# Kernel tuning notes

Hardware: AMD Instinct MI355X
Metric: run time of the kernel (lower is better)

Reference implementation:

```python
import jax, jax.numpy as jnp
import numpy as np

N = 50000          # nodes
E = 600000         # edges
D_IN = 256         # input_feat_dim
H1 = 128           # hidden_dim1
H2 = 64            # hidden_dim2
DK = 64            # trs_depth (total key/value depth)
HEADS = 2


def setup_inputs() -> dict:
    key = jax.random.key(0)
    ks = jax.random.split(key, 12)
    inp = {
        "ns_emb": jax.random.normal(ks[0], (N, D_IN), dtype=jnp.float32),
        "edge_rows": jax.random.randint(ks[1], (E,), 0, N, dtype=jnp.int32),
        "edge_cols": jax.random.randint(ks[2], (E,), 0, N, dtype=jnp.int32),
        "edge_vals": jax.random.uniform(ks[3], (E,), dtype=jnp.float32),
        "condition": jax.random.normal(ks[4], (1, 128, H1), dtype=jnp.float32),
        # GCN linear weights (bias=False), stored [in, out]
        "W_hidden": jax.random.normal(ks[5], (D_IN, H1), dtype=jnp.float32) / np.sqrt(D_IN),
        "W_mu": jax.random.normal(ks[6], (H1, H2), dtype=jnp.float32) / np.sqrt(H1),
        "W_var": jax.random.normal(ks[7], (H1, H2), dtype=jnp.float32) / np.sqrt(H1),
        # MultiHeadAttention (bias-free) projections
        "Wq": jax.random.normal(ks[8], (H1, DK), dtype=jnp.float32) / np.sqrt(H1),
        "Wk": jax.random.normal(ks[9], (H1, DK), dtype=jnp.float32) / np.sqrt(H1),
        "Wv": jax.random.normal(ks[10], (H1, DK), dtype=jnp.float32) / np.sqrt(H1),
        "Wo": jax.random.normal(ks[11], (DK, H1), dtype=jnp.float32) / np.sqrt(DK),
    }
    return inp


def _spmm(rows, cols, vals, x):
    # sparse [N,N] @ x  via gather + segment-sum over COO edges
    gathered = vals[:, None] * x[cols]            # [E, d]
    return jax.ops.segment_sum(gathered, rows, num_segments=N)


def _gcn(x, W, rows, cols, vals):
    # dropout is identity in eval mode
    support = jax.nn.leaky_relu(x @ W)            # [N, out]
    out = _spmm(rows, cols, vals, support)        # [N, out]
    return jax.nn.leaky_relu(out)


def _mha(q, kv, Wq, Wk, Wv, Wo):
    # MoEL-style MultiHeadAttention, bias-free, no mask/dropout
    B, Lq, _ = q.shape
    Lk = kv.shape[1]
    dk = DK // HEADS
    Q = (q @ Wq).reshape(B, Lq, HEADS, dk).transpose(0, 2, 1, 3) * (dk ** -0.5)
    K = (kv @ Wk).reshape(B, Lk, HEADS, dk).transpose(0, 2, 1, 3)
    V = (kv @ Wv).reshape(B, Lk, HEADS, dk).transpose(0, 2, 1, 3)
    logits = jnp.einsum("bhqd,bhkd->bhqk", Q, K)
    w = jax.nn.softmax(logits, axis=-1)
    ctx = jnp.einsum("bhqk,bhkd->bhqd", w, V)
    ctx = ctx.transpose(0, 2, 1, 3).reshape(B, Lq, DK)
    return ctx @ Wo, w


def reference(ns_emb, edge_rows, edge_cols, edge_vals, condition,
              W_hidden, W_mu, W_var, Wq, Wk, Wv, Wo):
    hidden = _gcn(ns_emb, W_hidden, edge_rows, edge_cols, edge_vals)   # [N, H1]
    attended, _ = _mha(hidden[None], condition, Wq, Wk, Wv, Wo)        # [1, N, H1]
    h = attended[0]
    mu = _gcn(h, W_mu, edge_rows, edge_cols, edge_vals)                # [N, H2]
    var = _gcn(h, W_var, edge_rows, edge_cols, edge_vals)              # [N, H2]
    return mu, var
```

## Files before the change

kernel.cpp:

```cpp
#include <hip/hip_runtime.h>
#include <hip/hip_bf16.h>
#include <cstdint>


typedef __attribute__((ext_vector_type(8))) short short8;
typedef __attribute__((ext_vector_type(4))) float f32x4;
typedef __attribute__((ext_vector_type(4))) unsigned short ushort4_t;

__device__ __forceinline__ unsigned short f2bf(float f) {
    unsigned int u = __builtin_bit_cast(unsigned int, f);
    u += 0x7fffu + ((u >> 16) & 1u);
    return (unsigned short)(u >> 16);
}
__device__ __forceinline__ float bf2f(unsigned short v) {
    return __builtin_bit_cast(float, (unsigned int)v << 16);
}


__global__ void hist_kernel(const int* __restrict__ rows, int* __restrict__ cnt, int E) {
    int i = blockIdx.x * blockDim.x + threadIdx.x;
    if (i < E) atomicAdd(&cnt[rows[i]], 1);
}

__global__ void scan1_kernel(const int* __restrict__ cnt, int* __restrict__ excl,
                             int* __restrict__ bsum, int N) {
    __shared__ int sh[256];
    int t = threadIdx.x;
    int i = blockIdx.x * 256 + t;
    int v = (i < N) ? cnt[i] : 0;
    sh[t] = v;
    __syncthreads();
    for (int off = 1; off < 256; off <<= 1) {
        int x = (t >= off) ? sh[t - off] : 0;
        __syncthreads();
        sh[t] += x;
        __syncthreads();
    }
    if (i < N) excl[i] = sh[t] - v;
    if (t == 255) bsum[blockIdx.x] = sh[255];
}

__global__ void scan23_kernel(const int* __restrict__ excl, const int* __restrict__ bsum,
                              int* __restrict__ row_start, int* __restrict__ cursor,
                              int nb, int N, int E) {
    __shared__ int sh[256];
    int t = threadIdx.x;
    int v = (t < nb) ? bsum[t] : 0;
    sh[t] = v;
    __syncthreads();
    for (int off = 1; off < 256; off <<= 1) {
        int x = (t >= off) ? sh[t - off] : 0;
        __syncthreads();
        sh[t] += x;
        __syncthreads();
    }
    int boff = (blockIdx.x > 0) ? sh[blockIdx.x - 1] : 0;
    int i = blockIdx.x * 256 + t;
    if (i < N) {
        int w = excl[i] + boff;
        row_start[i] = w;
        cursor[i] = w;
    }
    if (i == 0) row_start[N] = E;
}

__global__ void scatter_kernel(const int* __restrict__ rows, const int* __restrict__ colsIn,
                               const float* __restrict__ valsIn, int* __restrict__ cursor,
                               int2* __restrict__ pack, int E) {
    int i = blockIdx.x * blockDim.x + threadIdx.x;
    if (i < E) {
        int r = rows[i];
        int p = atomicAdd(&cursor[r], 1);
        pack[p] = make_int2(colsIn[i], __float_as_int(valsIn[i]));
    }
}


__global__ __launch_bounds__(256) void prep_kv_kernel(
    const float* __restrict__ Wh, const float* __restrict__ Wq,
    const float* __restrict__ Wo, const float* __restrict__ Wmu,
    const float* __restrict__ Wvar, const float* __restrict__ cond,
    const float* __restrict__ Wk, const float* __restrict__ Wv,
    unsigned short* __restrict__ WhT, unsigned short* __restrict__ WqT,
    unsigned short* __restrict__ WoT, unsigned short* __restrict__ WmuT,
    unsigned short* __restrict__ WvarT, unsigned short* __restrict__ Ktt,
    unsigned short* __restrict__ Vt)
{
    const int t = threadIdx.x;
    if (blockIdx.x < 256) {
        int idx = blockIdx.x * 256 + t;
        if (idx < 32768) {
            int n = idx & 127, k = idx >> 7;
            WhT[n * 256 + k] = f2bf(Wh[k * 128 + n]);
        } else if (idx < 40960) {
            int i = idx - 32768, n = i & 63, k = i >> 6;
            WqT[n * 128 + k] = f2bf(Wq[k * 64 + n]);
        } else if (idx < 49152) {
            int i = idx - 40960, n = i & 127, k = i >> 7;
            WoT[n * 64 + k] = f2bf(Wo[k * 128 + n]);
        } else if (idx < 57344) {
            int i = idx - 49152, n = i & 63, k = i >> 6;
            WmuT[n * 128 + k] = f2bf(Wmu[k * 64 + n]);
        } else if (idx < 65536) {
            int i = idx - 57344, n = i & 63, k = i >> 6;
            WvarT[n * 128 + k] = f2bf(Wvar[k * 64 + n]);
        }
    } else {
        int b2 = blockIdx.x - 256;
        __shared__ float c[2][128];
        c[t >> 7][t & 127] = cond[b2 * 256 + t];
        __syncthreads();
        int j = b2 * 2 + (t >> 7);
        int tl = t & 127;
        const float* W = (tl < 64) ? Wk : Wv;
        int col = tl & 63;
        float acc = 0.f;
#pragma unroll 8
        for (int k = 0; k < 128; ++k) acc = fmaf(c[t >> 7][k], W[k * 64 + col], acc);
        int h = col >> 5, d = col & 31;
        if (tl < 64) Ktt[((size_t)h * 128 + j) * 32 + d] = f2bf(acc * 0.17677669529663687f);
        else         Vt[((size_t)h * 32 + d) * 128 + j] = f2bf(acc);
    }
}


__global__ __launch_bounds__(256) void gcn1_gemm(
    const float* __restrict__ A, const unsigned short* __restrict__ BT,
    unsigned short* __restrict__ C, int M)
{
    __shared__ unsigned short As[128][72];
    __shared__ unsigned short Bs[128][72];

    const int tid = threadIdx.x;
    const int lane = tid & 63, wave = tid >> 6;
    const int wm = wave & 1, wn = wave >> 1;
    const int quad = lane >> 4, l16 = lane & 15;
    const int r0 = blockIdx.x * 128;

    f32x4 acc[4][4];
#pragma unroll
    for (int mt = 0; mt < 4; ++mt)
#pragma unroll
        for (int nt = 0; nt < 4; ++nt)
#pragma unroll
            for (int r = 0; r < 4; ++r) acc[mt][nt][r] = 0.f;

    for (int kc = 0; kc < 256; kc += 64) {
#pragma unroll
        for (int i = 0; i < 8; ++i) {
            int f = tid + 256 * i;
            int row = f >> 4, kq = (f & 15) << 2;
            int gr = r0 + row;
            if (gr >= M) gr = M - 1;
            float4 v = *reinterpret_cast<const float4*>(&A[(size_t)gr * 256 + kc + kq]);
            ushort4_t pv;
            pv[0] = f2bf(v.x); pv[1] = f2bf(v.y); pv[2] = f2bf(v.z); pv[3] = f2bf(v.w);
            *reinterpret_cast<ushort4_t*>(&As[row][kq]) = pv;
        }
#pragma unroll
        for (int i = 0; i < 4; ++i) {
            int f = tid + 256 * i;
            int n = f >> 3, k8 = (f & 7) << 3;
            *reinterpret_cast<short8*>(&Bs[n][k8]) =
                *reinterpret_cast<const short8*>(&BT[(size_t)n * 256 + kc + k8]);
        }
        __syncthreads();

#pragma unroll
        for (int ks = 0; ks < 2; ++ks) {
            const int koff = ks * 32 + quad * 8;
            short8 a[4], b[4];
#pragma unroll
            for (int mt = 0; mt < 4; ++mt)
                a[mt] = *reinterpret_cast<const short8*>(&As[wm * 64 + mt * 16 + l16][koff]);
#pragma unroll
            for (int nt = 0; nt < 4; ++nt)
                b[nt] = *reinterpret_cast<const short8*>(&Bs[wn * 64 + nt * 16 + l16][koff]);
#pragma unroll
            for (int mt = 0; mt < 4; ++mt)
#pragma unroll
                for (int nt = 0; nt < 4; ++nt)
                    acc[mt][nt] = __builtin_amdgcn_mfma_f32_16x16x32_bf16(
                        a[mt], b[nt], acc[mt][nt], 0, 0, 0);
        }
        __syncthreads();
    }

#pragma unroll
    for (int mt = 0; mt < 4; ++mt)
#pragma unroll
        for (int nt = 0; nt < 4; ++nt) {
            int gc = wn * 64 + nt * 16 + l16;
#pragma unroll
            for (int r = 0; r < 4; ++r) {
                int gr = r0 + wm * 64 + mt * 16 + quad * 4 + r;
                if (gr < M) {
                    float v = acc[mt][nt][r];
                    v = v > 0.f ? v : 0.01f * v;
                    C[(size_t)gr * 128 + gc] = f2bf(v);
                }
            }
        }
}


__global__ __launch_bounds__(256) void attn_muvar_kernel(
    const unsigned short* __restrict__ hidden,
    const unsigned short* __restrict__ WqT,
    const unsigned short* __restrict__ Ktt,
    const unsigned short* __restrict__ Vt,
    const unsigned short* __restrict__ WoT,
    const unsigned short* __restrict__ WmuT,
    const unsigned short* __restrict__ WvarT,
    unsigned short* __restrict__ muvar,
    int M)
{
    __shared__ unsigned short Ap[128 * 136];
    __shared__ unsigned short Bp[10240];
    __shared__ unsigned short Cp[128 * 72];
    __shared__ float redm[2][128];
    __shared__ float reds[2][128];

    const int tid = threadIdx.x;
    const int lane = tid & 63, wave = tid >> 6;
    const int wm = wave & 1, wn = wave >> 1;
    const int quad = lane >> 4, l16 = lane & 15;
    const int r0 = blockIdx.x * 128;

#pragma unroll
    for (int i = 0; i < 8; ++i) {
        int f = tid + 256 * i;
        int row = f >> 4, k8 = (f & 15) << 3;
        int gr = r0 + row;
        if (gr >= M) gr = M - 1;
        *reinterpret_cast<short8*>(&Ap[row * 136 + k8]) =
            *reinterpret_cast<const short8*>(&hidden[(size_t)gr * 128 + k8]);
    }
#pragma unroll
    for (int i = 0; i < 4; ++i) {
        int f = tid + 256 * i;
        int n = f >> 4, k8 = (f & 15) << 3;
        *reinterpret_cast<short8*>(&Bp[n * 136 + k8]) =
            *reinterpret_cast<const short8*>(&WqT[(size_t)n * 128 + k8]);
    }
    __syncthreads();

    {
        f32x4 accq[4][2];
#pragma unroll
        for (int mt = 0; mt < 4; ++mt)
#pragma unroll
            for (int nt = 0; nt < 2; ++nt)
#pragma unroll
                for (int r = 0; r < 4; ++r) accq[mt][nt][r] = 0.f;
#pragma unroll
        for (int ks = 0; ks < 4; ++ks) {
            const int koff = ks * 32 + quad * 8;
            short8 a[4], b[2];
#pragma unroll
            for (int mt = 0; mt < 4; ++mt)
                a[mt] = *reinterpret_cast<const short8*>(&Ap[(wm * 64 + mt * 16 + l16) * 136 + koff]);
#pragma unroll
            for (int nt = 0; nt < 2; ++nt)
                b[nt] = *reinterpret_cast<const short8*>(&Bp[(wn * 32 + nt * 16 + l16) * 136 + koff]);
#pragma unroll
            for (int mt = 0; mt < 4; ++mt)
#pragma unroll
                for (int nt = 0; nt < 2; ++nt)
                    accq[mt][nt] = __builtin_amdgcn_mfma_f32_16x16x32_bf16(
                        a[mt], b[nt], accq[mt][nt], 0, 0, 0);
        }
#pragma unroll
        for (int mt = 0; mt < 4; ++mt)
#pragma unroll
            for (int nt = 0; nt < 2; ++nt) {
                int col = wn * 32 + nt * 16 + l16;
#pragma unroll
                for (int r = 0; r < 4; ++r) {
                    int row = wm * 64 + mt * 16 + quad * 4 + r;
                    Cp[row * 72 + col] = f2bf(accq[mt][nt][r]);
                }
            }
    }
    __syncthreads();

    for (int h = 0; h < 2; ++h) {
#pragma unroll
        for (int i = 0; i < 2; ++i) {
            int f = tid + 256 * i;
            int key = f >> 2, d8 = (f & 3) << 3;
            *reinterpret_cast<short8*>(&Bp[key * 40 + d8]) =
                *reinterpret_cast<const short8*>(&Ktt[((size_t)h * 128 + key) * 32 + d8]);
        }
#pragma unroll
        for (int i = 0; i < 2; ++i) {
            int f = tid + 256 * i;
            int d = f >> 4, k8 = (f & 15) << 3;
            *reinterpret_cast<short8*>(&Bp[5120 + d * 136 + k8]) =
                *reinterpret_cast<const short8*>(&Vt[((size_t)h * 32 + d) * 128 + k8]);
        }
        __syncthreads();

        f32x4 accl[4][4];
        {
            short8 a[4], b[4];
#pragma unroll
            for (int mt = 0; mt < 4; ++mt)
                a[mt] = *reinterpret_cast<const short8*>(&Cp[(wm * 64 + mt * 16 + l16) * 72 + h * 32 + quad * 8]);
#pragma unroll
            for (int nt = 0; nt < 4; ++nt)
                b[nt] = *reinterpret_cast<const short8*>(&Bp[(wn * 64 + nt * 16 + l16) * 40 + quad * 8]);
#pragma unroll
            for (int mt = 0; mt < 4; ++mt)
#pragma unroll
                for (int nt = 0; nt < 4; ++nt) {
                    f32x4 z; z[0] = 0.f; z[1] = 0.f; z[2] = 0.f; z[3] = 0.f;
                    accl[mt][nt] = __builtin_amdgcn_mfma_f32_16x16x32_bf16(a[mt], b[nt], z, 0, 0, 0);
                }
        }

#pragma unroll
        for (int mt = 0; mt < 4; ++mt)
#pragma unroll
            for (int r = 0; r < 4; ++r) {
                float mx = fmaxf(fmaxf(accl[mt][0][r], accl[mt][1][r]),
                                 fmaxf(accl[mt][2][r], accl[mt][3][r]));
#pragma unroll
                for (int off = 1; off < 16; off <<= 1)
                    mx = fmaxf(mx, __shfl_xor(mx, off, 64));
                if (l16 == 0) redm[wn][wm * 64 + mt * 16 + quad * 4 + r] = mx;
            }
        __syncthreads();
#pragma unroll
        for (int mt = 0; mt < 4; ++mt)
#pragma unroll
            for (int r = 0; r < 4; ++r) {
                int lr = wm * 64 + mt * 16 + quad * 4 + r;
                float fm = fmaxf(redm[0][lr], redm[1][lr]);
                float s = 0.f;
#pragma unroll
                for (int nt = 0; nt < 4; ++nt) {
                    float e = __expf(accl[mt][nt][r] - fm);
                    accl[mt][nt][r] = e;
                    s += e;
                }
#pragma unroll
                for (int off = 1; off < 16; off <<= 1)
                    s += __shfl_xor(s, off, 64);
                if (l16 == 0) reds[wn][lr] = s;
            }
        __syncthreads();
#pragma unroll
        for (int mt = 0; mt < 4; ++mt)
#pragma unroll
            for (int r = 0; r < 4; ++r) {
                int lr = wm * 64 + mt * 16 + quad * 4 + r;
                float inv = 1.0f / (reds[0][lr] + reds[1][lr]);
#pragma unroll
                for (int nt = 0; nt < 4; ++nt)
                    Ap[lr * 136 + wn * 64 + nt * 16 + l16] = f2bf(accl[mt][nt][r] * inv);
            }
        __syncthreads();

        {
            f32x4 accc[4];
#pragma unroll
            for (int mt = 0; mt < 4; ++mt)
#pragma unroll
                for (int r = 0; r < 4; ++r) accc[mt][r] = 0.f;
#pragma unroll
            for (int ks = 0; ks < 4; ++ks) {
                const int koff = ks * 32 + quad * 8;
                short8 a[4];
#pragma unroll
                for (int mt = 0; mt < 4; ++mt)
                    a[mt] = *reinterpret_cast<const short8*>(&Ap[(wm * 64 + mt * 16 + l16) * 136 + koff]);
                short8 bb = *reinterpret_cast<const short8*>(&Bp[5120 + (wn * 16 + l16) * 136 + koff]);
#pragma unroll
                for (int mt = 0; mt < 4; ++mt)
                    accc[mt] = __builtin_amdgcn_mfma_f32_16x16x32_bf16(a[mt], bb, accc[mt], 0, 0, 0);
            }
#pragma unroll
            for (int mt = 0; mt < 4; ++mt)
#pragma unroll
                for (int r = 0; r < 4; ++r) {
                    int row = wm * 64 + mt * 16 + quad * 4 + r;
                    Cp[row * 72 + h * 32 + wn * 16 + l16] = f2bf(accc[mt][r]);
                }
        }
        __syncthreads();
    }

#pragma unroll
    for (int i = 0; i < 4; ++i) {
        int f = tid + 256 * i;
        int n = f >> 3, k8 = (f & 7) << 3;
        *reinterpret_cast<short8*>(&Bp[n * 72 + k8]) =
            *reinterpret_cast<const short8*>(&WoT[(size_t)n * 64 + k8]);
    }
    __syncthreads();
    {
        f32x4 acca[4][4];
#pragma unroll
        for (int mt = 0; mt < 4; ++mt)
#pragma unroll
            for (int nt = 0; nt < 4; ++nt)
#pragma unroll
                for (int r = 0; r < 4; ++r) acca[mt][nt][r] = 0.f;
#pragma unroll
        for (int ks = 0; ks < 2; ++ks) {
            const int koff = ks * 32 + quad * 8;
            short8 a[4], b[4];
#pragma unroll
            for (int mt = 0; mt < 4; ++mt)
                a[mt] = *reinterpret_cast<const short8*>(&Cp[(wm * 64 + mt * 16 + l16) * 72 + koff]);
#pragma unroll
            for (int nt = 0; nt < 4; ++nt)
                b[nt] = *reinterpret_cast<const short8*>(&Bp[(wn * 64 + nt * 16 + l16) * 72 + koff]);
#pragma unroll
            for (int mt = 0; mt < 4; ++mt)
#pragma unroll
                for (int nt = 0; nt < 4; ++nt)
                    acca[mt][nt] = __builtin_amdgcn_mfma_f32_16x16x32_bf16(
                        a[mt], b[nt], acca[mt][nt], 0, 0, 0);
        }
#pragma unroll
        for (int mt = 0; mt < 4; ++mt)
#pragma unroll
            for (int nt = 0; nt < 4; ++nt) {
                int col = wn * 64 + nt * 16 + l16;
#pragma unroll
                for (int r = 0; r < 4; ++r) {
                    int row = wm * 64 + mt * 16 + quad * 4 + r;
                    Ap[row * 136 + col] = f2bf(acca[mt][nt][r]);
                }
            }
    }
    __syncthreads();

    for (int half = 0; half < 2; ++half) {
        const unsigned short* WT = half ? WvarT : WmuT;
#pragma unroll
        for (int i = 0; i < 4; ++i) {
            int f = tid + 256 * i;
            int n = f >> 4, k8 = (f & 15) << 3;
            *reinterpret_cast<short8*>(&Bp[n * 136 + k8]) =
                *reinterpret_cast<const short8*>(&WT[(size_t)n * 128 + k8]);
        }
        __syncthreads();
        f32x4 accm[4][2];
#pragma unroll
        for (int mt = 0; mt < 4; ++mt)
#pragma unroll
            for (int nt = 0; nt < 2; ++nt)
#pragma unroll
                for (int r = 0; r < 4; ++r) accm[mt][nt][r] = 0.f;
#pragma unroll
        for (int ks = 0; ks < 4; ++ks) {
            const int koff = ks * 32 + quad * 8;
            short8 a[4], b[2];
#pragma unroll
            for (int mt = 0; mt < 4; ++mt)
                a[mt] = *reinterpret_cast<const short8*>(&Ap[(wm * 64 + mt * 16 + l16) * 136 + koff]);
#pragma unroll
            for (int nt = 0; nt < 2; ++nt)
                b[nt] = *reinterpret_cast<const short8*>(&Bp[(wn * 32 + nt * 16 + l16) * 136 + koff]);
#pragma unroll
            for (int mt = 0; mt < 4; ++mt)
#pragma unroll
                for (int nt = 0; nt < 2; ++nt)
                    accm[mt][nt] = __builtin_amdgcn_mfma_f32_16x16x32_bf16(
                        a[mt], b[nt], accm[mt][nt], 0, 0, 0);
        }
#pragma unroll
        for (int mt = 0; mt < 4; ++mt)
#pragma unroll
            for (int nt = 0; nt < 2; ++nt) {
                int gc = half * 64 + wn * 32 + nt * 16 + l16;
#pragma unroll
                for (int r = 0; r < 4; ++r) {
                    int gr = r0 + wm * 64 + mt * 16 + quad * 4 + r;
                    if (gr < M) {
                        float v = accm[mt][nt][r];
                        v = v > 0.f ? v : 0.01f * v;
                        muvar[(size_t)gr * 128 + gc] = f2bf(v);
                    }
                }
            }
        __syncthreads();
    }
}


template<bool SPLIT, typename OT>
__global__ __launch_bounds__(256) void spmm_kernel(
    const int* __restrict__ row_start, const int2* __restrict__ pack,
    const unsigned short* __restrict__ X,
    OT* __restrict__ out0, OT* __restrict__ out1, int N)
{
    const int wave = threadIdx.x >> 6, lane = threadIdx.x & 63;
    const int r = blockIdx.x * 4 + wave;
    if (r >= N) return;
    int s = __builtin_amdgcn_readfirstlane(row_start[r]);
    int e = __builtin_amdgcn_readfirstlane(row_start[r + 1]);
    const int fo = lane * 2;

    float ax[8], ay[8];
#pragma unroll
    for (int k = 0; k < 8; ++k) { ax[k] = 0.f; ay[k] = 0.f; }

    int i = s;
    for (; i + 8 <= e; i += 8) {
        int2 p[8];
        unsigned int x[8];
#pragma unroll
        for (int k = 0; k < 8; ++k) p[k] = pack[i + k];
#pragma unroll
        for (int k = 0; k < 8; ++k)
            x[k] = *reinterpret_cast<const unsigned int*>(&X[(size_t)p[k].x * 128 + fo]);
#pragma unroll
        for (int k = 0; k < 8; ++k) {
            float v = __int_as_float(p[k].y);
            ax[k] = fmaf(v, bf2f((unsigned short)x[k]), ax[k]);
            ay[k] = fmaf(v, bf2f((unsigned short)(x[k] >> 16)), ay[k]);
        }
    }
    if (i < e) {
        int2 p[8];
        unsigned int x[8];
#pragma unroll
        for (int k = 0; k < 8; ++k) {
            int idx = i + k;
            p[k] = pack[idx < e ? idx : e - 1];
        }
#pragma unroll
        for (int k = 0; k < 8; ++k)
            x[k] = *reinterpret_cast<const unsigned int*>(&X[(size_t)p[k].x * 128 + fo]);
#pragma unroll
        for (int k = 0; k < 8; ++k) {
            float v = (i + k < e) ? __int_as_float(p[k].y) : 0.f;
            ax[k] = fmaf(v, bf2f((unsigned short)x[k]), ax[k]);
            ay[k] = fmaf(v, bf2f((unsigned short)(x[k] >> 16)), ay[k]);
        }
    }

    float ox = ((ax[0] + ax[1]) + (ax[2] + ax[3])) + ((ax[4] + ax[5]) + (ax[6] + ax[7]));
    float oy = ((ay[0] + ay[1]) + (ay[2] + ay[3])) + ((ay[4] + ay[5]) + (ay[6] + ay[7]));
    ox = ox > 0.f ? ox : 0.01f * ox;
    oy = oy > 0.f ? oy : 0.01f * oy;

    if constexpr (!SPLIT) {
        unsigned int w = (unsigned int)f2bf(ox) | ((unsigned int)f2bf(oy) << 16);
        *reinterpret_cast<unsigned int*>(&out0[(size_t)r * 128 + fo]) = w;
    } else {
        if (lane < 32) {
            *reinterpret_cast<float2*>(&out0[(size_t)r * 64 + fo]) = make_float2(ox, oy);
        } else {
            *reinterpret_cast<float2*>(&out1[(size_t)r * 64 + (fo - 64)]) = make_float2(ox, oy);
        }
    }
}


extern "C" void kernel_launch(void* const* d_in, const int* in_sizes, int n_in,
                              void* d_out, int out_size, void* d_ws, size_t ws_size,
                              hipStream_t stream)
{
    const float* ns_emb   = (const float*)d_in[0];
    const int*   erows    = (const int*)d_in[1];
    const int*   ecols    = (const int*)d_in[2];
    const float* evals    = (const float*)d_in[3];
    const float* cond     = (const float*)d_in[4];
    const float* W_hidden = (const float*)d_in[5];
    const float* W_mu     = (const float*)d_in[6];
    const float* W_var    = (const float*)d_in[7];
    const float* Wq       = (const float*)d_in[8];
    const float* Wk       = (const float*)d_in[9];
    const float* Wv       = (const float*)d_in[10];
    const float* Wo       = (const float*)d_in[11];

    const int N = in_sizes[0] / 256;
    const int E = in_sizes[1];

    typedef unsigned short bf16;
    uint8_t* p = (uint8_t*)d_ws;
    auto alloc = [&](size_t bytes) {
        uint8_t* r = p;
        p += (bytes + 255) & ~(size_t)255;
        return r;
    };
    bf16* support1 = (bf16*)alloc(sizeof(bf16) * (size_t)N * 128);
    bf16* hidden   = (bf16*)alloc(sizeof(bf16) * (size_t)N * 128);
    bf16* muvarb   = (bf16*)alloc(sizeof(bf16) * (size_t)N * 128);
    bf16* Ktt      = (bf16*)alloc(sizeof(bf16) * 2 * 128 * 32);
    bf16* Vt       = (bf16*)alloc(sizeof(bf16) * 2 * 32 * 128);
    bf16* WhT      = (bf16*)alloc(sizeof(bf16) * 128 * 256);
    bf16* WqT      = (bf16*)alloc(sizeof(bf16) * 64 * 128);
    bf16* WoT      = (bf16*)alloc(sizeof(bf16) * 128 * 64);
    bf16* WmuT     = (bf16*)alloc(sizeof(bf16) * 64 * 128);
    bf16* WvarT    = (bf16*)alloc(sizeof(bf16) * 64 * 128);
    int*  cnt      = (int*)alloc(sizeof(int) * N);
    int*  excl     = (int*)alloc(sizeof(int) * N);
    int*  bsum     = (int*)alloc(sizeof(int) * 256);
    int*  row_start= (int*)alloc(sizeof(int) * (N + 1));
    int*  cursor   = (int*)alloc(sizeof(int) * N);
    int2* pack     = (int2*)alloc(sizeof(int2) * E);

    hipMemsetAsync(cnt, 0, sizeof(int) * N, stream);
    hist_kernel<<<(E + 255) / 256, 256, 0, stream>>>(erows, cnt, E);
    int nb = (N + 255) / 256;
    scan1_kernel<<<nb, 256, 0, stream>>>(cnt, excl, bsum, N);
    scan23_kernel<<<nb, 256, 0, stream>>>(excl, bsum, row_start, cursor, nb, N, E);
    scatter_kernel<<<(E + 255) / 256, 256, 0, stream>>>(erows, ecols, evals, cursor, pack, E);

    prep_kv_kernel<<<320, 256, 0, stream>>>(W_hidden, Wq, Wo, W_mu, W_var,
                                            cond, Wk, Wv,
                                            WhT, WqT, WoT, WmuT, WvarT, Ktt, Vt);

    const int mb = (N + 127) / 128;
    const int sblocks = (N + 3) / 4;

    gcn1_gemm<<<mb, 256, 0, stream>>>(ns_emb, WhT, support1, N);
    spmm_kernel<false, bf16><<<sblocks, 256, 0, stream>>>(
        row_start, pack, support1, hidden, nullptr, N);

    attn_muvar_kernel<<<mb, 256, 0, stream>>>(hidden, WqT, Ktt, Vt, WoT,
                                              WmuT, WvarT, muvarb, N);

    float* out = (float*)d_out;
    spmm_kernel<true, float><<<sblocks, 256, 0, stream>>>(
        row_start, pack, muvarb, out, out + (size_t)N * 64, N);
}
```

Baseline: 268.0 us.

## Fuse first SpMM into attention kernel and prefold Wo into Wmu/Wvar

The first sparse aggregation moves into the attention kernel, which gathers support1 rows directly into shared memory, so the hidden intermediate and its global round trip go away. Wo is precomputed into Wo·Wmu and Wo·Wvar in the prep kernel, turning the out-projection plus two mu/var GEMMs into a single 64→128 GEMM. The fp32→bf16 conversion in gcn1 now uses packed v_cvt_pk_bf16_f32 instructions. Risks: the fused kernel has only 391 blocks doing sequential per-row gathers (32 rows per wave), so parallelism drops compared with the per-row spmm launch, and folding the weights changes bf16 rounding.

```diff
diff --git a/kernel.cpp b/kernel.cpp
--- a/kernel.cpp
+++ b/kernel.cpp
@@ -78,35 +78,27 @@
 
 __global__ __launch_bounds__(256) void prep_kv_kernel(
     const float* __restrict__ Wh, const float* __restrict__ Wq,
+    const float* __restrict__ cond,
+    const float* __restrict__ Wk, const float* __restrict__ Wv,
     const float* __restrict__ Wo, const float* __restrict__ Wmu,
-    const float* __restrict__ Wvar, const float* __restrict__ cond,
-    const float* __restrict__ Wk, const float* __restrict__ Wv,
+    const float* __restrict__ Wvar,
     unsigned short* __restrict__ WhT, unsigned short* __restrict__ WqT,
-    unsigned short* __restrict__ WoT, unsigned short* __restrict__ WmuT,
-    unsigned short* __restrict__ WvarT, unsigned short* __restrict__ Ktt,
-    unsigned short* __restrict__ Vt)
+    unsigned short* __restrict__ Ktt, unsigned short* __restrict__ Vt,
+    unsigned short* __restrict__ WomT)
 {
     const int t = threadIdx.x;
-    if (blockIdx.x < 256) {
-        int idx = blockIdx.x * 256 + t;
+    const int bid = blockIdx.x;
+    if (bid < 160) {
+        int idx = bid * 256 + t;
         if (idx < 32768) {
             int n = idx & 127, k = idx >> 7;
             WhT[n * 256 + k] = f2bf(Wh[k * 128 + n]);
-        } else if (idx < 40960) {
+        } else {
             int i = idx - 32768, n = i & 63, k = i >> 6;
             WqT[n * 128 + k] = f2bf(Wq[k * 64 + n]);
-        } else if (idx < 49152) {
-            int i = idx - 40960, n = i & 127, k = i >> 7;
-            WoT[n * 64 + k] = f2bf(Wo[k * 128 + n]);
-        } else if (idx < 57344) {
-            int i = idx - 49152, n = i & 63, k = i >> 6;
-            WmuT[n * 128 + k] = f2bf(Wmu[k * 64 + n]);
-        } else if (idx < 65536) {
-            int i = idx - 57344, n = i & 63, k = i >> 6;
-            WvarT[n * 128 + k] = f2bf(Wvar[k * 64 + n]);
-        }
-    } else {
-        int b2 = blockIdx.x - 256;
+        }
+    } else if (bid < 224) {
+        int b2 = bid - 160;
         __shared__ float c[2][128];
         c[t >> 7][t & 127] = cond[b2 * 256 + t];
         __syncthreads();
@@ -120,6 +112,24 @@
         int h = col >> 5, d = col & 31;
         if (tl < 64) Ktt[((size_t)h * 128 + j) * 32 + d] = f2bf(acc * 0.17677669529663687f);
         else         Vt[((size_t)h * 32 + d) * 128 + j] = f2bf(acc);
+    } else {
+        int wb = bid - 224;
+        __shared__ float WoTl[128 * 65];
+#pragma unroll
+        for (int i = 0; i < 32; ++i) {
+            int idx = t + 256 * i;
+            int d = idx >> 7, k = idx & 127;
+            WoTl[k * 65 + d] = Wo[idx];
+        }
+        __syncthreads();
+        int o = wb * 256 + t;
+        int d = o & 63, n = o >> 6;
+        const float* W = (n < 64) ? Wmu : Wvar;
+        int j = n & 63;
+        float acc = 0.f;
+#pragma unroll 8
+        for (int k = 0; k < 128; ++k) acc = fmaf(WoTl[k * 65 + d], W[k * 64 + j], acc);
+        WomT[n * 64 + d] = f2bf(acc);
     }
 }
 
@@ -153,9 +163,10 @@
             int gr = r0 + row;
             if (gr >= M) gr = M - 1;
             float4 v = *reinterpret_cast<const float4*>(&A[(size_t)gr * 256 + kc + kq]);
-            ushort4_t pv;
-            pv[0] = f2bf(v.x); pv[1] = f2bf(v.y); pv[2] = f2bf(v.z); pv[3] = f2bf(v.w);
-            *reinterpret_cast<ushort4_t*>(&As[row][kq]) = pv;
+            unsigned int lo, hi;
+            asm("v_cvt_pk_bf16_f32 %0, %1, %2" : "=v"(lo) : "v"(v.x), "v"(v.y));
+            asm("v_cvt_pk_bf16_f32 %0, %1, %2" : "=v"(hi) : "v"(v.z), "v"(v.w));
+            *reinterpret_cast<uint2*>(&As[row][kq]) = make_uint2(lo, hi);
         }
 #pragma unroll
         for (int i = 0; i < 4; ++i) {
@@ -205,13 +216,13 @@
 
 
 __global__ __launch_bounds__(256) void attn_muvar_kernel(
-    const unsigned short* __restrict__ hidden,
+    const unsigned short* __restrict__ support1,
+    const int* __restrict__ row_start,
+    const int2* __restrict__ pack,
     const unsigned short* __restrict__ WqT,
     const unsigned short* __restrict__ Ktt,
     const unsigned short* __restrict__ Vt,
-    const unsigned short* __restrict__ WoT,
-    const unsigned short* __restrict__ WmuT,
-    const unsigned short* __restrict__ WvarT,
+    const unsigned short* __restrict__ WomT,
     unsigned short* __restrict__ muvar,
     int M)
 {
@@ -228,21 +239,80 @@
     const int r0 = blockIdx.x * 128;
 
 #pragma unroll
-    for (int i = 0; i < 8; ++i) {
-        int f = tid + 256 * i;
-        int row = f >> 4, k8 = (f & 15) << 3;
-        int gr = r0 + row;
-        if (gr >= M) gr = M - 1;
-        *reinterpret_cast<short8*>(&Ap[row * 136 + k8]) =
-            *reinterpret_cast<const short8*>(&hidden[(size_t)gr * 128 + k8]);
-    }
-#pragma unroll
     for (int i = 0; i < 4; ++i) {
         int f = tid + 256 * i;
         int n = f >> 4, k8 = (f & 15) << 3;
         *reinterpret_cast<short8*>(&Bp[n * 136 + k8]) =
             *reinterpret_cast<const short8*>(&WqT[(size_t)n * 128 + k8]);
     }
+
+    {
+        const int fo = lane * 2;
+        const int base = r0 + wave * 32;
+        const bool fast = (base + 32 <= M);
+        int bnds = 0;
+        if (fast && lane <= 32) bnds = row_start[base + lane];
+
+        for (int it = 0; it < 32; ++it) {
+            int row = wave * 32 + it;
+            int s, e;
+            if (fast) {
+                s = __shfl(bnds, it, 64);
+                e = __shfl(bnds, it + 1, 64);
+            } else {
+                int gr = r0 + row;
+                if (gr >= M) gr = M - 1;
+                s = __builtin_amdgcn_readfirstlane(row_start[gr]);
+                e = __builtin_amdgcn_readfirstlane(row_start[gr + 1]);
+            }
+
+            float ax[8], ay[8];
+#pragma unroll
+            for (int k = 0; k < 8; ++k) { ax[k] = 0.f; ay[k] = 0.f; }
+
+            int i = s;
+            for (; i + 8 <= e; i += 8) {
+                int2 p[8];
+                unsigned int x[8];
+#pragma unroll
+                for (int k = 0; k < 8; ++k) p[k] = pack[i + k];
+#pragma unroll
+                for (int k = 0; k < 8; ++k)
+                    x[k] = *reinterpret_cast<const unsigned int*>(&support1[(size_t)p[k].x * 128 + fo]);
+#pragma unroll
+                for (int k = 0; k < 8; ++k) {
+                    float v = __int_as_float(p[k].y);
+                    ax[k] = fmaf(v, bf2f((unsigned short)x[k]), ax[k]);
+                    ay[k] = fmaf(v, bf2f((unsigned short)(x[k] >> 16)), ay[k]);
+                }
+            }
+            if (i < e) {
+                int2 p[8];
+                unsigned int x[8];
+#pragma unroll
+                for (int k = 0; k < 8; ++k) {
+                    int idx = i + k;
+                    p[k] = pack[idx < e ? idx : e - 1];
+                }
+#pragma unroll
+                for (int k = 0; k < 8; ++k)
+                    x[k] = *reinterpret_cast<const unsigned int*>(&support1[(size_t)p[k].x * 128 + fo]);
+#pragma unroll
+                for (int k = 0; k < 8; ++k) {
+                    float v = (i + k < e) ? __int_as_float(p[k].y) : 0.f;
+                    ax[k] = fmaf(v, bf2f((unsigned short)x[k]), ax[k]);
+                    ay[k] = fmaf(v, bf2f((unsigned short)(x[k] >> 16)), ay[k]);
+                }
+            }
+
+            float ox = ((ax[0] + ax[1]) + (ax[2] + ax[3])) + ((ax[4] + ax[5]) + (ax[6] + ax[7]));
+            float oy = ((ay[0] + ay[1]) + (ay[2] + ay[3])) + ((ay[4] + ay[5]) + (ay[6] + ay[7]));
+            ox = ox > 0.f ? ox : 0.01f * ox;
+            oy = oy > 0.f ? oy : 0.01f * oy;
+            unsigned int w = (unsigned int)f2bf(ox) | ((unsigned int)f2bf(oy) << 16);
+            *reinterpret_cast<unsigned int*>(&Ap[row * 136 + fo]) = w;
+        }
+    }
     __syncthreads();
 
     {
@@ -396,17 +466,17 @@
         int f = tid + 256 * i;
         int n = f >> 3, k8 = (f & 7) << 3;
         *reinterpret_cast<short8*>(&Bp[n * 72 + k8]) =
-            *reinterpret_cast<const short8*>(&WoT[(size_t)n * 64 + k8]);
+            *reinterpret_cast<const short8*>(&WomT[(size_t)n * 64 + k8]);
     }
     __syncthreads();
     {
-        f32x4 acca[4][4];
+        f32x4 accf[4][4];
 #pragma unroll
         for (int mt = 0; mt < 4; ++mt)
 #pragma unroll
             for (int nt = 0; nt < 4; ++nt)
 #pragma unroll
-                for (int r = 0; r < 4; ++r) acca[mt][nt][r] = 0.f;
+                for (int r = 0; r < 4; ++r) accf[mt][nt][r] = 0.f;
 #pragma unroll
         for (int ks = 0; ks < 2; ++ks) {
             const int koff = ks * 32 + quad * 8;
@@ -421,73 +491,24 @@
             for (int mt = 0; mt < 4; ++mt)
 #pragma unroll
                 for (int nt = 0; nt < 4; ++nt)
-                    acca[mt][nt] = __builtin_amdgcn_mfma_f32_16x16x32_bf16(
-                        a[mt], b[nt], acca[mt][nt], 0, 0, 0);
+                    accf[mt][nt] = __builtin_amdgcn_mfma_f32_16x16x32_bf16(
+                        a[mt], b[nt], accf[mt][nt], 0, 0, 0);
         }
 #pragma unroll
         for (int mt = 0; mt < 4; ++mt)
 #pragma unroll
             for (int nt = 0; nt < 4; ++nt) {
-                int col = wn * 64 + nt * 16 + l16;
-#pragma unroll
-                for (int r = 0; r < 4; ++r) {
-                    int row = wm * 64 + mt * 16 + quad * 4 + r;
-                    Ap[row * 136 + col] = f2bf(acca[mt][nt][r]);
-                }
-            }
-    }
-    __syncthreads();
-
-    for (int half = 0; half < 2; ++half) {
-        const unsigned short* WT = half ? WvarT : WmuT;
-#pragma unroll
-        for (int i = 0; i < 4; ++i) {
-            int f = tid + 256 * i;
-            int n = f >> 4, k8 = (f & 15) << 3;
-            *reinterpret_cast<short8*>(&Bp[n * 136 + k8]) =
-                *reinterpret_cast<const short8*>(&WT[(size_t)n * 128 + k8]);
-        }
-        __syncthreads();
-        f32x4 accm[4][2];
-#pragma unroll
-        for (int mt = 0; mt < 4; ++mt)
-#pragma unroll
-            for (int nt = 0; nt < 2; ++nt)
-#pragma unroll
-                for (int r = 0; r < 4; ++r) accm[mt][nt][r] = 0.f;
-#pragma unroll
-        for (int ks = 0; ks < 4; ++ks) {
-            const int koff = ks * 32 + quad * 8;
-            short8 a[4], b[2];
-#pragma unroll
-            for (int mt = 0; mt < 4; ++mt)
-                a[mt] = *reinterpret_cast<const short8*>(&Ap[(wm * 64 + mt * 16 + l16) * 136 + koff]);
-#pragma unroll
-            for (int nt = 0; nt < 2; ++nt)
-                b[nt] = *reinterpret_cast<const short8*>(&Bp[(wn * 32 + nt * 16 + l16) * 136 + koff]);
-#pragma unroll
-            for (int mt = 0; mt < 4; ++mt)
-#pragma unroll
-                for (int nt = 0; nt < 2; ++nt)
-                    accm[mt][nt] = __builtin_amdgcn_mfma_f32_16x16x32_bf16(
-                        a[mt], b[nt], accm[mt][nt], 0, 0, 0);
-        }
-#pragma unroll
-        for (int mt = 0; mt < 4; ++mt)
-#pragma unroll
-            for (int nt = 0; nt < 2; ++nt) {
-                int gc = half * 64 + wn * 32 + nt * 16 + l16;
+                int gc = wn * 64 + nt * 16 + l16;
 #pragma unroll
                 for (int r = 0; r < 4; ++r) {
                     int gr = r0 + wm * 64 + mt * 16 + quad * 4 + r;
                     if (gr < M) {
-                        float v = accm[mt][nt][r];
+                        float v = accf[mt][nt][r];
                         v = v > 0.f ? v : 0.01f * v;
                         muvar[(size_t)gr * 128 + gc] = f2bf(v);
                     }
                 }
             }
-        __syncthreads();
     }
 }
 
@@ -590,15 +611,12 @@
         return r;
     };
     bf16* support1 = (bf16*)alloc(sizeof(bf16) * (size_t)N * 128);
-    bf16* hidden   = (bf16*)alloc(sizeof(bf16) * (size_t)N * 128);
     bf16* muvarb   = (bf16*)alloc(sizeof(bf16) * (size_t)N * 128);
     bf16* Ktt      = (bf16*)alloc(sizeof(bf16) * 2 * 128 * 32);
     bf16* Vt       = (bf16*)alloc(sizeof(bf16) * 2 * 32 * 128);
     bf16* WhT      = (bf16*)alloc(sizeof(bf16) * 128 * 256);
     bf16* WqT      = (bf16*)alloc(sizeof(bf16) * 64 * 128);
-    bf16* WoT      = (bf16*)alloc(sizeof(bf16) * 128 * 64);
-    bf16* WmuT     = (bf16*)alloc(sizeof(bf16) * 64 * 128);
-    bf16* WvarT    = (bf16*)alloc(sizeof(bf16) * 64 * 128);
+    bf16* WomT     = (bf16*)alloc(sizeof(bf16) * 128 * 64);
     int*  cnt      = (int*)alloc(sizeof(int) * N);
     int*  excl     = (int*)alloc(sizeof(int) * N);
     int*  bsum     = (int*)alloc(sizeof(int) * 256);
@@ -613,19 +631,17 @@
     scan23_kernel<<<nb, 256, 0, stream>>>(excl, bsum, row_start, cursor, nb, N, E);
     scatter_kernel<<<(E + 255) / 256, 256, 0, stream>>>(erows, ecols, evals, cursor, pack, E);
 
-    prep_kv_kernel<<<320, 256, 0, stream>>>(W_hidden, Wq, Wo, W_mu, W_var,
-                                            cond, Wk, Wv,
-                                            WhT, WqT, WoT, WmuT, WvarT, Ktt, Vt);
+    prep_kv_kernel<<<256, 256, 0, stream>>>(W_hidden, Wq, cond, Wk, Wv,
+                                            Wo, W_mu, W_var,
+                                            WhT, WqT, Ktt, Vt, WomT);
 
     const int mb = (N + 127) / 128;
     const int sblocks = (N + 3) / 4;
 
     gcn1_gemm<<<mb, 256, 0, stream>>>(ns_emb, WhT, support1, N);
-    spmm_kernel<false, bf16><<<sblocks, 256, 0, stream>>>(
-        row_start, pack, support1, hidden, nullptr, N);
-
-    attn_muvar_kernel<<<mb, 256, 0, stream>>>(hidden, WqT, Ktt, Vt, WoT,
-                                              WmuT, WvarT, muvarb, N);
+
+    attn_muvar_kernel<<<mb, 256, 0, stream>>>(support1, row_start, pack,
+                                              WqT, Ktt, Vt, WomT, muvarb, N);
 
     float* out = (float*)d_out;
     spmm_kernel<true, float><<<sblocks, 256, 0, stream>>>(
```

After: 301.4 us. 1.12x slower.
